# Kernel tuning notes

Measured on AMD Instinct MI355X. Metric: run time of the kernel, lower is better.

The kernel has to match this reference:

```python
import jax, jax.numpy as jnp
import numpy as np

IN_FEATURES = 64
OUT_FEATURES = 64

def setup_inputs() -> dict:
    key = jax.random.key(0)
    kx, kw = jax.random.split(key)
    x = jax.random.normal(kx, (32, 32, 32, IN_FEATURES), dtype=jnp.float32)
    # quadratic weight: [out_features, in_features * in_features]
    W = jax.random.normal(kw, (OUT_FEATURES, IN_FEATURES * IN_FEATURES), dtype=jnp.float32) * 0.02
    return {"x": x, "W": W}

def reference(x, W):
    # Original: outer = x[..., :, None] * x[..., None, :] -> [B,D1,D2,F*F]; then linear(W).
    # Equivalent fused bilinear contraction: out_o = sum_{f,g} x_f x_g W_{o,f,g}
    F_ = x.shape[-1]
    Wr = W.reshape(W.shape[0], F_, F_)  # [O, F, F]
    return jnp.einsum('bacf,bacg,ofg->baco', x, x, Wr)
```

## Files before the change

kernel.cpp:

```cpp
#include <hip/hip_runtime.h>

typedef __attribute__((ext_vector_type(8))) short bf16x8;
typedef __attribute__((ext_vector_type(4))) float f32x4;

constexpr int KPK = 2304;
constexpr int QK  = 576;
constexpr int NROUND = 9;

__device__ __forceinline__ unsigned short bf_rne(float f) {
  unsigned u = __float_as_uint(f);
  return (unsigned short)((u + 0x7fffu + ((u >> 16) & 1u)) >> 16);
}

__global__ __launch_bounds__(256) void wprep_kernel(const float* __restrict__ W,
                                                    unsigned short* __restrict__ Wp) {
  int e = blockIdx.x * 256 + threadIdx.x;
  int o = e / KPK;
  int k = e - o * KPK;
  int kq = k / QK;
  int r = k - kq * QK;
  int j = r >> 6, i = r & 63;
  int run1 = 8 - kq;
  int G, F;
  if (j < run1) { G = 7 - kq; F = j; } else { G = kq; F = j - run1; }
  int f = F * 8 + (i >> 3), g = G * 8 + (i & 7);
  float v = W[o * 4096 + f * 64 + g];
  if (F != G) v += W[o * 4096 + g * 64 + f];
  Wp[o * KPK + k] = bf_rne(v);
}

__global__ __launch_bounds__(256, 2) void quad_kernel(const float* __restrict__ x,
                                                      const unsigned short* __restrict__ Wp,
                                                      float* __restrict__ out) {
  __shared__ alignas(16) unsigned short Ws[2][4][4096];
  __shared__ alignas(16) float xT[4096];

  const int t = threadIdx.x;
  const int lane = t & 63;
  const int kq = t >> 6;
  const int q = lane >> 4;
  const int r16 = lane & 15;
  const int pxbase = blockIdx.x * 64;

  auto stage = [&](int j, int buf) {
    char* ldsbase = reinterpret_cast<char*>(&Ws[buf][0][0]) + kq * 1024;
    const char* wp = reinterpret_cast<const char*>(Wp) + j * 128;
    const int o0 = t >> 3;
    const int o1 = 32 + o0;
    const int ib = (t & 7) * 16;
    const int s0 = o0 * 4608 + (ib ^ ((o0 & 7) << 4));
    const int s1 = o1 * 4608 + (ib ^ ((o1 & 7) << 4));
#pragma unroll
    for (int i = 0; i < 8; ++i) {
      int src_off = ((i & 1) ? s1 : s0) + (i >> 1) * 1152;
      __builtin_amdgcn_global_load_lds(
          (const __attribute__((address_space(1))) void*)(wp + src_off),
          (__attribute__((address_space(3))) void*)(ldsbase + i * 4096), 16, 0, 0);
    }
  };

  stage(0, 0);

  {
    const float* xg_ = x + (long)pxbase * 64;
#pragma unroll
    for (int c = 0; c < 4; ++c) {
      int e = c * 256 + t;
      int px = e >> 4;
      int f0 = (e & 15) * 4;
      float4 v = *reinterpret_cast<const float4*>(xg_ + px * 64 + f0);
      xT[(f0 + 0) * 64 + (px ^ (f0 + 0))] = v.x;
      xT[(f0 + 1) * 64 + (px ^ (f0 + 1))] = v.y;
      xT[(f0 + 2) * 64 + (px ^ (f0 + 2))] = v.z;
      xT[(f0 + 3) * 64 + (px ^ (f0 + 3))] = v.w;
    }
  }
  __syncthreads();

  float xg[4][8];
  auto load_xg = [&](int G) {
#pragma unroll
    for (int m = 0; m < 4; ++m) {
      int px = m * 16 + r16;
#pragma unroll
      for (int b = 0; b < 8; ++b) {
        int row = G * 8 + b;
        xg[m][b] = xT[row * 64 + (px ^ row)];
      }
    }
  };
  const int run1 = 8 - kq;
  load_xg(7 - kq);

  f32x4 acc[4][4] = {};
  int buf = 0;
  for (int j = 0; j < NROUND; ++j) {
    if (j) __syncthreads();
    if (j + 1 < NROUND) stage(j + 1, buf ^ 1);
    const int F = (j < run1) ? j : j - run1;
    if (j == run1) load_xg(kq);

    float xf[4][2];
#pragma unroll
    for (int m = 0; m < 4; ++m) {
      int px = m * 16 + r16;
#pragma unroll
      for (int s = 0; s < 2; ++s) {
        int row = F * 8 + s * 4 + q;
        xf[m][s] = xT[row * 64 + (px ^ row)];
      }
    }

    const char* wsb = reinterpret_cast<const char*>(&Ws[buf][kq][0]);
#pragma unroll
    for (int s = 0; s < 2; ++s) {
      bf16x8 afr[4];
#pragma unroll
      for (int m = 0; m < 4; ++m) {
        union { unsigned u[4]; bf16x8 v; } pk;
#pragma unroll
        for (int i = 0; i < 4; ++i) {
          unsigned p0 = __float_as_uint(xf[m][s] * xg[m][2 * i]);
          unsigned p1 = __float_as_uint(xf[m][s] * xg[m][2 * i + 1]);
          pk.u[i] = __builtin_amdgcn_perm(p1, p0, 0x07060302u);
        }
        afr[m] = pk.v;
      }
#pragma unroll
      for (int nt = 0; nt < 4; ++nt) {
        int o = nt * 16 + r16;
        bf16x8 bfr = *reinterpret_cast<const bf16x8*>(
            wsb + o * 128 + ((s * 64 + q * 16) ^ ((o & 7) << 4)));
#pragma unroll
        for (int m = 0; m < 4; ++m)
          acc[m][nt] = __builtin_amdgcn_mfma_f32_16x16x32_bf16(afr[m], bfr, acc[m][nt], 0, 0, 0);
      }
    }
    buf ^= 1;
  }

  __syncthreads();
  float* red = reinterpret_cast<float*>(&Ws[0][0][0]);
#pragma unroll
  for (int m = 0; m < 4; ++m) {
#pragma unroll
    for (int nt = 0; nt < 4; ++nt) {
      *reinterpret_cast<f32x4*>(red + (m * 4 + kq) * 1024 + (nt * 16 + r16) * 16 + q * 4) =
          acc[m][nt];
    }
  }
  __syncthreads();
  {
    const float* base = red + kq * 4 * 1024;
#pragma unroll
    for (int nt = 0; nt < 4; ++nt) {
      int off = (nt * 16 + r16) * 16 + q * 4;
      f32x4 ssum = *reinterpret_cast<const f32x4*>(base + off);
#pragma unroll
      for (int w = 1; w < 4; ++w)
        ssum += *reinterpret_cast<const f32x4*>(base + w * 1024 + off);
      long prow = pxbase + kq * 16 + q * 4;
#pragma unroll
      for (int b = 0; b < 4; ++b)
        out[(prow + b) * 64 + nt * 16 + r16] = ssum[b];
    }
  }
}

extern "C" void kernel_launch(void* const* d_in, const int* in_sizes, int n_in,
                              void* d_out, int out_size, void* d_ws, size_t ws_size,
                              hipStream_t stream) {
  const float* x = (const float*)d_in[0];
  const float* W = (const float*)d_in[1];
  float* out = (float*)d_out;
  unsigned short* Wp = (unsigned short*)d_ws;

  hipLaunchKernelGGL(wprep_kernel, dim3(576), dim3(256), 0, stream, W, Wp);
  hipLaunchKernelGGL(quad_kernel, dim3(512), dim3(256), 0, stream, x, Wp, out);
}
```

Measured before the change: 25.91 us.

## Replace block-wide double buffer with per-wave triple-buffered weight ring and vmcnt waits

```diff
diff --git a/kernel.cpp b/kernel.cpp
--- a/kernel.cpp
+++ b/kernel.cpp
@@ -5,7 +5,7 @@
 
 constexpr int KPK = 2304;
 constexpr int QK  = 576;
-constexpr int NROUND = 9;
+constexpr int NCH = 18;
 
 __device__ __forceinline__ unsigned short bf_rne(float f) {
   unsigned u = __float_as_uint(f);
@@ -32,8 +32,8 @@
 __global__ __launch_bounds__(256, 2) void quad_kernel(const float* __restrict__ x,
                                                       const unsigned short* __restrict__ Wp,
                                                       float* __restrict__ out) {
-  __shared__ alignas(16) unsigned short Ws[2][4][4096];
-  __shared__ alignas(16) float xT[4096];
+  __shared__ alignas(16) char smem[65536];
+  float* xT = reinterpret_cast<float*>(smem);
 
   const int t = threadIdx.x;
   const int lane = t & 63;
@@ -42,24 +42,24 @@
   const int r16 = lane & 15;
   const int pxbase = blockIdx.x * 64;
 
-  auto stage = [&](int j, int buf) {
-    char* ldsbase = reinterpret_cast<char*>(&Ws[buf][0][0]) + kq * 1024;
-    const char* wp = reinterpret_cast<const char*>(Wp) + j * 128;
-    const int o0 = t >> 3;
-    const int o1 = 32 + o0;
-    const int ib = (t & 7) * 16;
-    const int s0 = o0 * 4608 + (ib ^ ((o0 & 7) << 4));
-    const int s1 = o1 * 4608 + (ib ^ ((o1 & 7) << 4));
+  char* ring = smem + 16384 + kq * 12288;
+
+  const char* wsrc = reinterpret_cast<const char*>(Wp) +
+                     (lane >> 2) * (KPK * 2) + (lane & 3) * 16 + kq * (QK * 2);
+
+  auto issue = [&](int c, int slot) {
+    const char* s = wsrc + c * 64;
+    char* d = ring + slot * 4096;
 #pragma unroll
-    for (int i = 0; i < 8; ++i) {
-      int src_off = ((i & 1) ? s1 : s0) + (i >> 1) * 1152;
+    for (int i = 0; i < 4; ++i) {
       __builtin_amdgcn_global_load_lds(
-          (const __attribute__((address_space(1))) void*)(wp + src_off),
-          (__attribute__((address_space(3))) void*)(ldsbase + i * 4096), 16, 0, 0);
+          (const __attribute__((address_space(1))) void*)(s + i * (16 * KPK * 2)),
+          (__attribute__((address_space(3))) void*)(d + i * 1024), 16, 0, 0);
     }
   };
 
-  stage(0, 0);
+  issue(0, 0);
+  issue(1, 1);
 
   {
     const float* xg_ = x + (long)pxbase * 64;
@@ -93,65 +93,62 @@
   load_xg(7 - kq);
 
   f32x4 acc[4][4] = {};
-  int buf = 0;
-  for (int j = 0; j < NROUND; ++j) {
-    if (j) __syncthreads();
-    if (j + 1 < NROUND) stage(j + 1, buf ^ 1);
-    const int F = (j < run1) ? j : j - run1;
-    if (j == run1) load_xg(kq);
+  int slot = 0;
 
-    float xf[4][2];
+  for (int j = 0; j < NCH; ++j) {
+    int islot = slot + 2 - ((slot >= 1) ? 3 : 0);
+    if (j + 2 < NCH) issue(j + 2, islot);
+
+    if (j < NCH - 2)       asm volatile("s_waitcnt vmcnt(8)" ::: "memory");
+    else if (j == NCH - 2) asm volatile("s_waitcnt vmcnt(4)" ::: "memory");
+    else                   asm volatile("s_waitcnt vmcnt(0)" ::: "memory");
+
+    const int s = j & 1;
+    const int blk = j >> 1;
+    const int F = (blk < run1) ? blk : blk - run1;
+    if (j == 2 * run1) load_xg(kq);
+
+    const char* wb = ring + slot * 4096;
+    bf16x8 bfr[4];
+#pragma unroll
+    for (int nt = 0; nt < 4; ++nt)
+      bfr[nt] = *reinterpret_cast<const bf16x8*>(wb + (nt * 16 + r16) * 64 + q * 16);
+
+    const int row = F * 8 + s * 4 + q;
+    bf16x8 afr[4];
 #pragma unroll
     for (int m = 0; m < 4; ++m) {
-      int px = m * 16 + r16;
+      float xf = xT[row * 64 + ((m * 16 + r16) ^ row)];
+      union { unsigned u[4]; bf16x8 v; } pk;
 #pragma unroll
-      for (int s = 0; s < 2; ++s) {
-        int row = F * 8 + s * 4 + q;
-        xf[m][s] = xT[row * 64 + (px ^ row)];
+      for (int i = 0; i < 4; ++i) {
+        unsigned p0 = __float_as_uint(xf * xg[m][2 * i]);
+        unsigned p1 = __float_as_uint(xf * xg[m][2 * i + 1]);
+        pk.u[i] = __builtin_amdgcn_perm(p1, p0, 0x07060302u);
       }
+      afr[m] = pk.v;
     }
 
-    const char* wsb = reinterpret_cast<const char*>(&Ws[buf][kq][0]);
 #pragma unroll
-    for (int s = 0; s < 2; ++s) {
-      bf16x8 afr[4];
+    for (int nt = 0; nt < 4; ++nt)
 #pragma unroll
-      for (int m = 0; m < 4; ++m) {
-        union { unsigned u[4]; bf16x8 v; } pk;
-#pragma unroll
-        for (int i = 0; i < 4; ++i) {
-          unsigned p0 = __float_as_uint(xf[m][s] * xg[m][2 * i]);
-          unsigned p1 = __float_as_uint(xf[m][s] * xg[m][2 * i + 1]);
-          pk.u[i] = __builtin_amdgcn_perm(p1, p0, 0x07060302u);
-        }
-        afr[m] = pk.v;
-      }
-#pragma unroll
-      for (int nt = 0; nt < 4; ++nt) {
-        int o = nt * 16 + r16;
-        bf16x8 bfr = *reinterpret_cast<const bf16x8*>(
-            wsb + o * 128 + ((s * 64 + q * 16) ^ ((o & 7) << 4)));
-#pragma unroll
-        for (int m = 0; m < 4; ++m)
-          acc[m][nt] = __builtin_amdgcn_mfma_f32_16x16x32_bf16(afr[m], bfr, acc[m][nt], 0, 0, 0);
-      }
-    }
-    buf ^= 1;
+      for (int m = 0; m < 4; ++m)
+        acc[m][nt] = __builtin_amdgcn_mfma_f32_16x16x32_bf16(afr[m], bfr[nt], acc[m][nt], 0, 0, 0);
+
+    slot = (slot == 2) ? 0 : slot + 1;
   }
 
   __syncthreads();
-  float* red = reinterpret_cast<float*>(&Ws[0][0][0]);
+  float* red = reinterpret_cast<float*>(smem);
 #pragma unroll
-  for (int m = 0; m < 4; ++m) {
+  for (int m = 0; m < 4; ++m)
 #pragma unroll
-    for (int nt = 0; nt < 4; ++nt) {
+    for (int nt = 0; nt < 4; ++nt)
       *reinterpret_cast<f32x4*>(red + (m * 4 + kq) * 1024 + (nt * 16 + r16) * 16 + q * 4) =
           acc[m][nt];
-    }
-  }
   __syncthreads();
   {
-    const float* base = red + kq * 4 * 1024;
+    const float* base = red + kq * 4096;
 #pragma unroll
     for (int nt = 0; nt < 4; ++nt) {
       int off = (nt * 16 + r16) * 16 + q * 4;
```

Measured after the change: 26.34 us. No clear change (+1.7%).
